# Kernel tuning notes

Measured on AMD Instinct MI355X. Metric: run time of the kernel, lower is better.

## Reference

```python
import jax, jax.numpy as jnp
import numpy as np

S = 17          # grid size = 544/32
A = 5           # num anchors
C = 20          # num classes
B = 256         # batch
G = 32          # GT boxes per image (distinct cells, sorted)
HW = S * S
IOU_THRESH = 0.6
OBJ_SCALE, NOOBJ_SCALE, COORD_SCALE, CLS_SCALE = 5.0, 1.0, 1.0, 1.0
ANCHORS = np.array([[1.3221, 1.73145], [3.19275, 4.00944], [5.05587, 8.09892],
                    [9.47112, 4.84053], [11.2364, 10.0071]], dtype=np.float32)


def setup_inputs() -> dict:
    key = jax.random.key(0)
    k1, k2, k3 = jax.random.split(key, 3)
    bbox_pred = jax.random.uniform(k1, (B, HW, A, 4), dtype=jnp.float32)
    iou_pred = jax.random.uniform(k2, (B, HW, A, 1), dtype=jnp.float32)
    score_pred = jax.random.uniform(k3, (B, HW, A, C), dtype=jnp.float32)
    # Structured targets: per image, G GT boxes in G distinct cells, sorted by
    # linear cell index (matches the implicit assumption of the torch code
    # that pairs sorted true-cells with GT-ordered anchor indices).
    rng = np.random.default_rng(0)
    tg = np.zeros((B, G, 6), np.float32)
    for b in range(B):
        cells = np.sort(rng.permutation(HW)[:G])
        ci, cj = cells // S, cells % S
        u = rng.uniform(0.2, 0.8, (G, 2))
        cx = (ci + u[:, 0]) / S
        cy = (cj + u[:, 1]) / S
        w = rng.uniform(0.05, 0.25, G).astype(np.float32)
        h = rng.uniform(0.05, 0.25, G).astype(np.float32)
        tg[b, :, 0] = b
        tg[b, :, 1] = rng.integers(0, C, G)
        tg[b, :, 2] = cx - w / 2
        tg[b, :, 3] = cy - h / 2
        tg[b, :, 4] = cx + w / 2
        tg[b, :, 5] = cy + h / 2
    return {"bbox_pred": bbox_pred, "iou_pred": iou_pred, "score_pred": score_pred,
            "targets": jnp.asarray(tg.reshape(B * G, 6)),
            "anchors": jnp.asarray(ANCHORS)}


def _box_iou(a, b):
    # a: [N,4], b: [G,4] corner boxes -> [N,G]
    lt = jnp.maximum(a[:, None, :2], b[None, :, :2])
    rb = jnp.minimum(a[:, None, 2:], b[None, :, 2:])
    wh = jnp.clip(rb - lt, 0.0)
    inter = wh[..., 0] * wh[..., 1]
    area_a = (a[:, 2] - a[:, 0]) * (a[:, 3] - a[:, 1])
    area_b = (b[:, 2] - b[:, 0]) * (b[:, 3] - b[:, 1])
    return inter / (area_a[:, None] + area_b[None, :] - inter)


def _forward(bbox_pred, iou_pred, score_pred, targets, anchors):
    anc = anchors / 17.0
    # decode predicted boxes: xy offset + cell index, wh scaled by anchors
    gi, gj = jnp.meshgrid(jnp.arange(S), jnp.arange(S), indexing="ij")
    c_map = jnp.stack([gi, gj], axis=-1).astype(bbox_pred.dtype)[None, :, :, None, :]
    p5 = bbox_pred.reshape(B, S, S, A, 4)
    xy = (p5[..., :2] + c_map) / S
    wh = p5[..., 2:] * anc[None, None, None] / S
    c_box = jnp.concatenate([xy, wh], axis=-1).reshape(B, HW * A, 4)
    pred_b = jnp.concatenate([c_box[..., :2] - c_box[..., 2:] / 2,
                              c_box[..., :2] + c_box[..., 2:] / 2], axis=-1)
    tgt = targets.reshape(B, G, 6)

    def per_image(bbox_p, iou_p, score_p, pb, t):
        gt_class = t[:, 1].astype(jnp.int32)
        gt_box = t[:, 2:]                               # corner, normalized
        gt_cxy = (gt_box[:, :2] + gt_box[:, 2:]) / 2    # b_box_to_c_box
        gt_wh = gt_box[:, 2:] - gt_box[:, :2]
        c_xy = gt_cxy * S
        c_ij = jnp.floor(c_xy).astype(jnp.int32)
        offset_xy = c_xy - c_ij
        tar_gt_box = jnp.concatenate([offset_xy, gt_wh], axis=-1)
        # distinct+sorted cells by construction -> dedup keeps all G boxes
        cells = c_ij[:, 0] * S + c_ij[:, 1]             # [G]
        iou = _box_iou(pb, gt_box)                      # [HW*A, G]
        best_iou = iou.max(axis=1).reshape(HW, A, 1)
        iou_mask = jnp.where(best_iou <= IOU_THRESH, NOOBJ_SCALE * (0.0 - iou_p), 0.0)
        # anchor wh vs gt wh IoU -> best anchor per GT
        inter = (jnp.minimum(anc[:, None, 0], gt_wh[None, :, 0]) *
                 jnp.minimum(anc[:, None, 1], gt_wh[None, :, 1]))
        a_area = anc[:, 0] * anc[:, 1]
        g_area = gt_wh[:, 0] * gt_wh[:, 1]
        anchor_iou = inter / (a_area[:, None] + g_area[None, :] - inter)
        anchor_index = anchor_iou.argmax(axis=0)        # [G]
        iou3 = iou.reshape(HW, A, G)
        gidx = jnp.arange(G)
        iou_mask = iou_mask.at[cells, anchor_index, 0].set(
            OBJ_SCALE * (1.0 - iou_p[cells, anchor_index, 0]))
        iou_t = jnp.zeros((HW, A, 1), bbox_p.dtype).at[cells, anchor_index, 0].set(
            iou3[cells, anchor_index, gidx])
        box_mask = jnp.full((HW, A, 1), 0.01, bbox_p.dtype).at[cells, anchor_index, 0].set(COORD_SCALE)
        boxes_t = jnp.concatenate([jnp.full((HW, A, 2), 0.5, bbox_p.dtype),
                                   jnp.ones((HW, A, 2), bbox_p.dtype)], axis=-1)
        boxes_t = boxes_t.at[cells, anchor_index].set(tar_gt_box)
        class_mask = jnp.zeros((HW, A, 1), bbox_p.dtype).at[cells, anchor_index, 0].set(CLS_SCALE)
        class_t = jnp.zeros((HW, A, C), bbox_p.dtype).at[cells, anchor_index, gt_class].set(1.0)
        box_l = jnp.sum((bbox_p * box_mask - boxes_t * box_mask) ** 2) / G
        iou_l = jnp.sum((iou_p * iou_mask - iou_t * iou_mask) ** 2) / G
        cls_l = jnp.sum((score_p * class_mask - class_t * class_mask) ** 2) / G
        return box_l + iou_l + cls_l

    return jnp.sum(jax.vmap(per_image)(bbox_pred, iou_pred, score_pred, pred_b, tgt))


def reference(bbox_pred, iou_pred, score_pred, targets, anchors):
    return _forward(bbox_pred, iou_pred, score_pred, targets, anchors)
```

## Files before the change

### kernel.cpp

```cpp
#include <hip/hip_runtime.h>

#define SS 17
#define AA 5
#define CC 20
#define BATCH 256
#define GG 32
#define HWC (SS * SS)
#define NP (HWC * AA)
#define SPLIT 8
#define CHUNK 181
#define NTHREADS 192
#define NPART (BATCH * SPLIT)
#define RTHREADS 256
#define INV_G (1.0f / 32.0f)

__global__ __launch_bounds__(NTHREADS) void yolo_loss_kernel(
    const float* __restrict__ bbox,
    const float* __restrict__ ioup,
    const float* __restrict__ score,
    const float* __restrict__ tgt,
    const float* __restrict__ anchors,
    float* __restrict__ part)
{
    const int b   = blockIdx.x;
    const int spl = blockIdx.y;
    const int tid = threadIdx.x;

    __shared__ float4 gbox[GG];
    __shared__ float4 tarb[GG];
    __shared__ int    gcls[GG];
    __shared__ float  anc[AA][2];
    __shared__ alignas(16) short assign[NP + 11];
    __shared__ float  wsum[NTHREADS / 64];

    const int pbase = spl * CHUNK;
    const int pend  = min(NP, pbase + CHUNK);
    const int gbase = b * NP;
    const int p     = pbase + tid;
    const bool valid = (p < pend);
    const int pc    = valid ? p : pbase;
    float4 bb = ((const float4*)bbox)[gbase + pc];
    float  ip = ioup[gbase + pc];

    {
        int2* ap = (int2*)assign;
        #pragma unroll
        for (int k = tid; k < 364; k += NTHREADS)
            ap[k] = make_int2(-1, -1);
    }
    if (tid < AA * 2) ((float*)anc)[tid] = anchors[tid] * (1.0f / 17.0f);
    __syncthreads();

    if (tid < GG) {
        const float* t = tgt + (size_t)(b * GG + tid) * 6;
        int   cls = (int)t[1];
        float x1 = t[2], y1 = t[3], x2 = t[4], y2 = t[5];
        float cx = (x1 + x2) * 0.5f, cy = (y1 + y2) * 0.5f;
        float gw = x2 - x1, gh = y2 - y1;
        float cxs = cx * (float)SS, cys = cy * (float)SS;
        int ci = (int)floorf(cxs), cj = (int)floorf(cys);
        gbox[tid] = make_float4(x1, y1, x2, y2);
        tarb[tid] = make_float4(cxs - (float)ci, cys - (float)cj, gw, gh);
        gcls[tid] = cls;
        float best = -1.0f; int bi = 0;
        for (int a = 0; a < AA; a++) {
            float aw = anc[a][0], ah = anc[a][1];
            float inter = fminf(aw, gw) * fminf(ah, gh);
            float v = inter / (aw * ah + gw * gh - inter);
            if (v > best) { best = v; bi = a; }
        }
        assign[(ci * SS + cj) * AA + bi] = (short)tid;
    }
    __syncthreads();

    float px1, py1, px2, py2, pa;
    {
        int hw = pc / AA, a = pc - hw * AA;
        int i = hw / SS,  j = hw - i * SS;
        float px = (bb.x + (float)i) * (1.0f / SS);
        float py = (bb.y + (float)j) * (1.0f / SS);
        float pw = bb.z * anc[a][0] * (1.0f / SS);
        float ph = bb.w * anc[a][1] * (1.0f / SS);
        px1 = px - pw * 0.5f; py1 = py - ph * 0.5f;
        px2 = px + pw * 0.5f; py2 = py + ph * 0.5f;
        pa  = (px2 - px1) * (py2 - py1);
    }

    float anyhit = -1.0f;
    #pragma unroll 8
    for (int g = 0; g < GG; g++) {
        float4 gb = gbox[g];
        float garea = (gb.z - gb.x) * (gb.w - gb.y);
        float w = fminf(px2, gb.z) - fmaxf(px1, gb.x);
        float h = fminf(py2, gb.w) - fmaxf(py1, gb.y);
        float inter = fmaxf(w, 0.0f) * fmaxf(h, 0.0f);
        anyhit = fmaxf(anyhit, __builtin_fmaf(-0.375f, pa + garea, inter));
    }

    float acc = 0.0f;
    if (valid) {
        int ga = (int)assign[p];
        if (ga >= 0) {
            float4 gb = gbox[ga];
            float w = fmaxf(fminf(px2, gb.z) - fmaxf(px1, gb.x), 0.0f);
            float h = fmaxf(fminf(py2, gb.w) - fmaxf(py1, gb.y), 0.0f);
            float inter = w * h;
            float garea = (gb.z - gb.x) * (gb.w - gb.y);
            float iou_t = inter / (pa + garea - inter);
            float4 tb = tarb[ga];
            float dx = bb.x - tb.x, dy = bb.y - tb.y;
            float dw = bb.z - tb.z, dh = bb.w - tb.w;
            acc += dx * dx + dy * dy + dw * dw + dh * dh;
            float m = 5.0f * (1.0f - ip);
            float d = ip - iou_t;
            acc += (m * m) * (d * d);
            const float4* sp4 = (const float4*)(score + (size_t)(gbase + p) * CC);
            int cls = gcls[ga];
            #pragma unroll
            for (int c4 = 0; c4 < CC / 4; c4++) {
                float4 sv = sp4[c4];
                float v0 = sv.x - (4 * c4 + 0 == cls ? 1.0f : 0.0f);
                float v1 = sv.y - (4 * c4 + 1 == cls ? 1.0f : 0.0f);
                float v2 = sv.z - (4 * c4 + 2 == cls ? 1.0f : 0.0f);
                float v3 = sv.w - (4 * c4 + 3 == cls ? 1.0f : 0.0f);
                acc += v0 * v0 + v1 * v1 + v2 * v2 + v3 * v3;
            }
        } else {
            float dx = bb.x - 0.5f, dy = bb.y - 0.5f;
            float dw = bb.z - 1.0f, dh = bb.w - 1.0f;
            acc += 1e-4f * (dx * dx + dy * dy + dw * dw + dh * dh);
            if (anyhit <= 0.0f) { float q = ip * ip; acc += q * q; }
        }
    }

    #pragma unroll
    for (int off = 32; off > 0; off >>= 1)
        acc += __shfl_down(acc, off, 64);
    if ((tid & 63) == 0) wsum[tid >> 6] = acc;
    __syncthreads();
    if (tid == 0)
        part[b * SPLIT + spl] = wsum[0] + wsum[1] + wsum[2];
}

__global__ __launch_bounds__(RTHREADS) void yolo_reduce_kernel(
    const float* __restrict__ part, float* __restrict__ out)
{
    const int tid = threadIdx.x;
    __shared__ float wsum[RTHREADS / 64];
    float s = 0.0f;
    #pragma unroll
    for (int k = 0; k < NPART / RTHREADS; k++)
        s += part[k * RTHREADS + tid];
    #pragma unroll
    for (int off = 32; off > 0; off >>= 1)
        s += __shfl_down(s, off, 64);
    if ((tid & 63) == 0) wsum[tid >> 6] = s;
    __syncthreads();
    if (tid == 0)
        out[0] = (wsum[0] + wsum[1] + wsum[2] + wsum[3]) * INV_G;
}

extern "C" void kernel_launch(void* const* d_in, const int* in_sizes, int n_in,
                              void* d_out, int out_size, void* d_ws, size_t ws_size,
                              hipStream_t stream) {
    const float* bbox    = (const float*)d_in[0];
    const float* ioup    = (const float*)d_in[1];
    const float* score   = (const float*)d_in[2];
    const float* tgt     = (const float*)d_in[3];
    const float* anchors = (const float*)d_in[4];
    float* out  = (float*)d_out;
    float* part = (float*)d_ws;

    dim3 grid(BATCH, SPLIT);
    yolo_loss_kernel<<<grid, NTHREADS, 0, stream>>>(bbox, ioup, score, tgt,
                                                    anchors, part);
    yolo_reduce_kernel<<<1, RTHREADS, 0, stream>>>(part, out);
}
```

Before: 94.25 us.

## Process three predictions per thread and read GT boxes via uniform loads

Reduces the grid from 8 to 2 splits per image, with 256 threads each handling 3 predictions. Per-image setup (assign init, GT decode, shared syncs) is amortized over more work. The GT loop now reads boxes from global memory with a uniform address so they can go through scalar loads, and it reuses each box for 3 predictions. In exchange there are fewer blocks (512), more registers per thread and less parallelism to hide latency.

New measurement: 89.22 us. 5.3% less time.

```diff
diff --git a/kernel.cpp b/kernel.cpp
--- a/kernel.cpp
+++ b/kernel.cpp
@@ -7,9 +7,10 @@
 #define GG 32
 #define HWC (SS * SS)
 #define NP (HWC * AA)
-#define SPLIT 8
-#define CHUNK 181
-#define NTHREADS 192
+#define SPLIT 2
+#define CHUNK 723
+#define NTHREADS 256
+#define NITEMS 3
 #define NPART (BATCH * SPLIT)
 #define RTHREADS 256
 #define INV_G (1.0f / 32.0f)
@@ -36,11 +37,19 @@
     const int pbase = spl * CHUNK;
     const int pend  = min(NP, pbase + CHUNK);
     const int gbase = b * NP;
-    const int p     = pbase + tid;
-    const bool valid = (p < pend);
-    const int pc    = valid ? p : pbase;
-    float4 bb = ((const float4*)bbox)[gbase + pc];
-    float  ip = ioup[gbase + pc];
+
+    int  p[NITEMS], pcl[NITEMS];
+    bool val[NITEMS];
+    float4 bb[NITEMS];
+    float  ip[NITEMS];
+    #pragma unroll
+    for (int k = 0; k < NITEMS; k++) {
+        p[k]   = pbase + tid + k * NTHREADS;
+        val[k] = (p[k] < pend);
+        pcl[k] = val[k] ? p[k] : pbase;
+        bb[k]  = ((const float4*)bbox)[gbase + pcl[k]];
+        ip[k]  = ioup[gbase + pcl[k]];
+    }
 
     {
         int2* ap = (int2*)assign;
@@ -73,48 +82,61 @@
     }
     __syncthreads();
 
-    float px1, py1, px2, py2, pa;
-    {
-        int hw = pc / AA, a = pc - hw * AA;
-        int i = hw / SS,  j = hw - i * SS;
-        float px = (bb.x + (float)i) * (1.0f / SS);
-        float py = (bb.y + (float)j) * (1.0f / SS);
-        float pw = bb.z * anc[a][0] * (1.0f / SS);
-        float ph = bb.w * anc[a][1] * (1.0f / SS);
-        px1 = px - pw * 0.5f; py1 = py - ph * 0.5f;
-        px2 = px + pw * 0.5f; py2 = py + ph * 0.5f;
-        pa  = (px2 - px1) * (py2 - py1);
-    }
-
-    float anyhit = -1.0f;
+    float px1[NITEMS], py1[NITEMS], px2[NITEMS], py2[NITEMS];
+    float pa[NITEMS], c375[NITEMS];
+    #pragma unroll
+    for (int k = 0; k < NITEMS; k++) {
+        int hw = pcl[k] / AA, a = pcl[k] - hw * AA;
+        int i = hw / SS,      j = hw - i * SS;
+        float px = (bb[k].x + (float)i) * (1.0f / SS);
+        float py = (bb[k].y + (float)j) * (1.0f / SS);
+        float pw = bb[k].z * anc[a][0] * (1.0f / SS);
+        float ph = bb[k].w * anc[a][1] * (1.0f / SS);
+        px1[k] = px - pw * 0.5f; py1[k] = py - ph * 0.5f;
+        px2[k] = px + pw * 0.5f; py2[k] = py + ph * 0.5f;
+        pa[k]  = (px2[k] - px1[k]) * (py2[k] - py1[k]);
+        c375[k] = 0.375f * pa[k];
+    }
+
+    const float* tg = tgt + (size_t)b * GG * 6;
+    float anyhit[NITEMS];
+    #pragma unroll
+    for (int k = 0; k < NITEMS; k++) anyhit[k] = -1.0f;
+
     #pragma unroll 8
     for (int g = 0; g < GG; g++) {
-        float4 gb = gbox[g];
-        float garea = (gb.z - gb.x) * (gb.w - gb.y);
-        float w = fminf(px2, gb.z) - fmaxf(px1, gb.x);
-        float h = fminf(py2, gb.w) - fmaxf(py1, gb.y);
-        float inter = fmaxf(w, 0.0f) * fmaxf(h, 0.0f);
-        anyhit = fmaxf(anyhit, __builtin_fmaf(-0.375f, pa + garea, inter));
+        float x1 = tg[g * 6 + 2], y1 = tg[g * 6 + 3];
+        float x2 = tg[g * 6 + 4], y2 = tg[g * 6 + 5];
+        float s375 = 0.375f * ((x2 - x1) * (y2 - y1));
+        #pragma unroll
+        for (int k = 0; k < NITEMS; k++) {
+            float w = fminf(px2[k], x2) - fmaxf(px1[k], x1);
+            float h = fminf(py2[k], y2) - fmaxf(py1[k], y1);
+            float inter = fmaxf(w, 0.0f) * fmaxf(h, 0.0f);
+            anyhit[k] = fmaxf(anyhit[k], inter - (s375 + c375[k]));
+        }
     }
 
     float acc = 0.0f;
-    if (valid) {
-        int ga = (int)assign[p];
+    #pragma unroll
+    for (int k = 0; k < NITEMS; k++) {
+        if (!val[k]) continue;
+        int ga = (int)assign[p[k]];
         if (ga >= 0) {
             float4 gb = gbox[ga];
-            float w = fmaxf(fminf(px2, gb.z) - fmaxf(px1, gb.x), 0.0f);
-            float h = fmaxf(fminf(py2, gb.w) - fmaxf(py1, gb.y), 0.0f);
+            float w = fmaxf(fminf(px2[k], gb.z) - fmaxf(px1[k], gb.x), 0.0f);
+            float h = fmaxf(fminf(py2[k], gb.w) - fmaxf(py1[k], gb.y), 0.0f);
             float inter = w * h;
             float garea = (gb.z - gb.x) * (gb.w - gb.y);
-            float iou_t = inter / (pa + garea - inter);
+            float iou_t = inter / (pa[k] + garea - inter);
             float4 tb = tarb[ga];
-            float dx = bb.x - tb.x, dy = bb.y - tb.y;
-            float dw = bb.z - tb.z, dh = bb.w - tb.w;
+            float dx = bb[k].x - tb.x, dy = bb[k].y - tb.y;
+            float dw = bb[k].z - tb.z, dh = bb[k].w - tb.w;
             acc += dx * dx + dy * dy + dw * dw + dh * dh;
-            float m = 5.0f * (1.0f - ip);
-            float d = ip - iou_t;
+            float m = 5.0f * (1.0f - ip[k]);
+            float d = ip[k] - iou_t;
             acc += (m * m) * (d * d);
-            const float4* sp4 = (const float4*)(score + (size_t)(gbase + p) * CC);
+            const float4* sp4 = (const float4*)(score + (size_t)(gbase + p[k]) * CC);
             int cls = gcls[ga];
             #pragma unroll
             for (int c4 = 0; c4 < CC / 4; c4++) {
@@ -126,10 +148,10 @@
                 acc += v0 * v0 + v1 * v1 + v2 * v2 + v3 * v3;
             }
         } else {
-            float dx = bb.x - 0.5f, dy = bb.y - 0.5f;
-            float dw = bb.z - 1.0f, dh = bb.w - 1.0f;
+            float dx = bb[k].x - 0.5f, dy = bb[k].y - 0.5f;
+            float dw = bb[k].z - 1.0f, dh = bb[k].w - 1.0f;
             acc += 1e-4f * (dx * dx + dy * dy + dw * dw + dh * dh);
-            if (anyhit <= 0.0f) { float q = ip * ip; acc += q * q; }
+            if (anyhit[k] <= 0.0f) { float q = ip[k] * ip[k]; acc += q * q; }
         }
     }
 
@@ -139,7 +161,7 @@
     if ((tid & 63) == 0) wsum[tid >> 6] = acc;
     __syncthreads();
     if (tid == 0)
-        part[b * SPLIT + spl] = wsum[0] + wsum[1] + wsum[2];
+        part[b * SPLIT + spl] = wsum[0] + wsum[1] + wsum[2] + wsum[3];
 }
 
 __global__ __launch_bounds__(RTHREADS) void yolo_reduce_kernel(
```
